# Kernel optimization log

Hardware: AMD Instinct MI355X
Metric: run time of the kernel (lower is better)

The kernel has to match this reference:

```python
import jax, jax.numpy as jnp
import numpy as np
from jax import lax

EPS = 1e-5
DN = ('NCHW', 'OIHW', 'NCHW')

def _sign(v):
    # (v >= 0) * 2 - 1
    return jnp.where(v >= 0, 1.0, -1.0).astype(v.dtype)

def _conv(x, w, b):
    y = lax.conv_general_dilated(x, w, (1, 1), 'VALID', dimension_numbers=DN)
    return y + b[None, :, None, None]

def _bn(x):
    # BatchNorm2d(affine=False), training mode: biased batch stats over (N,H,W)
    m = jnp.mean(x, axis=(0, 2, 3), keepdims=True)
    v = jnp.var(x, axis=(0, 2, 3), keepdims=True)
    return (x - m) * lax.rsqrt(v + EPS)

def setup_inputs() -> dict:
    key = jax.random.key(0)
    ks = jax.random.split(key, 9)
    f = jnp.float32
    B = 8192
    x = jax.random.normal(ks[0], (B, 1, 28, 28), dtype=f)
    # conv params, clipped to [-1, 1] as in clip_weights()
    w1 = jnp.clip(jax.random.normal(ks[1], (32, 1, 9, 9), dtype=f) * 0.1, -1, 1)
    b1 = jnp.clip(jax.random.normal(ks[2], (32,), dtype=f) * 0.1, -1, 1)
    w2 = jnp.clip(jax.random.normal(ks[3], (16, 32, 9, 9), dtype=f) * 0.1, -1, 1)
    b2 = jnp.clip(jax.random.normal(ks[4], (16,), dtype=f) * 0.1, -1, 1)
    w3 = jnp.clip(jax.random.normal(ks[5], (8, 16, 9, 9), dtype=f) * 0.1, -1, 1)
    b3 = jnp.clip(jax.random.normal(ks[6], (8,), dtype=f) * 0.1, -1, 1)
    wl = jnp.clip(jax.random.normal(ks[7], (10, 8, 4, 4), dtype=f) * 0.1, -1, 1)
    bl = jnp.clip(jax.random.normal(ks[8], (10,), dtype=f) * 0.1, -1, 1)
    return {"x": x, "w1": w1, "b1": b1, "w2": w2, "b2": b2,
            "w3": w3, "b3": b3, "wl": wl, "bl": bl}

def _block(x, w, b, act=True, norm=True, binarized=True):
    if binarized:
        w, b = _sign(w), _sign(b)
    x = _conv(x, w, b)
    if norm:
        x = _bn(x)
    if act:
        x = _sign(x) if binarized else jax.nn.relu(x)
    return x

def reference(x, w1, b1, w2, b2, w3, b3, wl, bl):
    x = _sign(x)                        # binarize input activations
    x = _block(x, w1, b1)               # (B, 32, 20, 20)
    x = _block(x, w2, b2)               # (B, 16, 12, 12)
    x = _block(x, w3, b3)               # (B,  8,  4,  4)
    x = _block(x, wl, bl, act=False, norm=False)  # (B, 10, 1, 1), binarized weights
    return x.reshape(-1, 10)
```

## Files before the change

### kernel.cpp

```cpp
#include <hip/hip_runtime.h>
#include <stdint.h>

#define BATCH 8192

#define OFF_W1R3   0
#define OFF_W2P    384
#define OFF_W3P    6144
#define OFF_WLB    9600
#define OFF_SBL    9760
#define OFF_TTOT   9856
#define OFF_S3     10184
#define OFF_S2PART 10496
#define OFF_Z2     76800
#define OFF_Z3     37825792

__global__ __launch_bounds__(256) void k1_pack_tsum(const float* __restrict__ x,
                                                    const float* __restrict__ w1,
                                                    const float* __restrict__ w2,
                                                    const float* __restrict__ w3,
                                                    const float* __restrict__ wl,
                                                    const float* __restrict__ bl,
                                                    uint8_t* __restrict__ ws) {
  int* Ttot = (int*)(ws + OFF_TTOT);
  const int tid = threadIdx.x;

  if (blockIdx.x == 0) {
    uint32_t* W1R3 = (uint32_t*)(ws + OFF_W1R3);
    uint32_t* W2P  = (uint32_t*)(ws + OFF_W2P);
    uint32_t* W3P  = (uint32_t*)(ws + OFF_W3P);
    uint64_t* WLB  = (uint64_t*)(ws + OFF_WLB);
    float*    SBL  = (float*)(ws + OFF_SBL);
    for (int e = tid; e < 96; e += 256) {
      int oc = e / 3, i = e % 3;
      uint32_t m = 0;
      for (int rr = 0; rr < 3; ++rr)
        for (int kw = 0; kw < 9; ++kw)
          if (w1[oc*81 + (3*i+rr)*9 + kw] < 0.f) m |= 1u << (rr*9 + kw);
      W1R3[e] = m;
    }
    for (int e = tid; e < 648; e += 256) {
      int och = e / 81, k = e % 81;
      int kh = k / 9, kw = k % 9;
      uint32_t m0 = 0, m1 = 0;
      int oc0 = och*2;
      for (int ic = 0; ic < 32; ++ic) {
        if (w2[(oc0*32 + ic)*81 + k] < 0.f)     m0 |= 1u << ic;
        if (w2[((oc0+1)*32 + ic)*81 + k] < 0.f) m1 |= 1u << ic;
      }
      int idx = ((och*9 + kh)*10 + kw)*2;
      W2P[idx] = m0; W2P[idx+1] = m1;
    }
    for (int e = tid; e < 72; e += 256) {
      int idx = (e*10 + 9)*2;
      W2P[idx] = 0; W2P[idx+1] = 0;
    }
    for (int e = tid; e < 648; e += 256) {
      int oc = e / 81, k = e % 81;
      int kh = k / 9, kw = k % 9;
      uint32_t m = 0;
      for (int ic = 0; ic < 16; ++ic)
        if (w3[(oc*16 + ic)*81 + k] < 0.f) m |= 1u << ic;
      W3P[(oc*9 + kh)*12 + kw] = m;
    }
    for (int e = tid; e < 216; e += 256) {
      int row = e / 3, p = e % 3;
      W3P[row*12 + 9 + p] = 0;
    }
    for (int e = tid; e < 20; e += 256) {
      int oc = e >> 1, word = e & 1;
      uint64_t m = 0;
      for (int b = 0; b < 64; ++b)
        if (wl[oc*128 + word*64 + b] < 0.f) m |= 1ull << b;
      WLB[e] = m;
    }
    if (tid < 10) SBL[tid] = (bl[tid] >= 0.f) ? 1.f : -1.f;
  }

  __shared__ uint32_t rowm[896];
  __shared__ int Tacc[81];
  if (tid < 81) Tacc[tid] = 0;
  __syncthreads();

  const int img0 = blockIdx.x * 32;
  #pragma unroll
  for (int it = 0; it < 4; ++it) {
    int R = tid + it*256;
    if (R < 896) {
      int il = R / 28, r = R % 28;
      const float4* xr = (const float4*)(x + (size_t)(img0 + il) * 784 + r * 28);
      uint32_t m = 0;
      #pragma unroll
      for (int j = 0; j < 7; ++j) {
        float4 v = xr[j];
        if (v.x < 0.f) m |= 1u << (j*4+0);
        if (v.y < 0.f) m |= 1u << (j*4+1);
        if (v.z < 0.f) m |= 1u << (j*4+2);
        if (v.w < 0.f) m |= 1u << (j*4+3);
      }
      rowm[R] = m;
    }
  }
  __syncthreads();

  for (int T = tid; T < 288; T += 256) {
    int il = T / 9, kw = T % 9;
    int base = il * 28;
    int n9[9];
    int sum20 = 0;
    #pragma unroll
    for (int r = 0; r < 20; ++r) {
      int n = __popc((rowm[base + r] >> kw) & 0xFFFFFu);
      if (r < 9) n9[r] = n;
      sum20 += n;
    }
    atomicAdd(&Tacc[kw], 400 - 2*sum20);
    #pragma unroll
    for (int kh = 1; kh <= 8; ++kh) {
      int nadd = __popc((rowm[base + kh + 19] >> kw) & 0xFFFFFu);
      sum20 += nadd - n9[kh-1];
      atomicAdd(&Tacc[kh*9 + kw], 400 - 2*sum20);
    }
  }
  __syncthreads();
  if (tid < 81) atomicAdd(&Ttot[tid], Tacc[tid]);
}

#define K2_IMGS 8
__global__ __launch_bounds__(256) void k2_conv12(const float* __restrict__ x,
                                                 uint8_t* __restrict__ ws) {
  const uint32_t* W1R3g = (const uint32_t*)(ws + OFF_W1R3);
  const uint32_t* W2Pg  = (const uint32_t*)(ws + OFF_W2P);
  const int* Ttot = (const int*)(ws + OFF_TTOT);
  int* S2P = (int*)(ws + OFF_S2PART);

  __shared__ uint32_t __attribute__((aligned(16))) rowm[K2_IMGS*28];
  __shared__ uint32_t __attribute__((aligned(16))) w1r3[96];
  __shared__ uint32_t __attribute__((aligned(16))) w2p[1440];
  __shared__ int tlds[81];
  __shared__ int t1s[32];
  __shared__ uint32_t __attribute__((aligned(16))) A1s[K2_IMGS*400];
  __shared__ int s2acc[16];

  const int tid = threadIdx.x;
  const int img0 = blockIdx.x * K2_IMGS;

  for (int e = tid; e < 96; e += 256)   w1r3[e] = W1R3g[e];
  for (int e = tid; e < 1440; e += 256) w2p[e]  = W2Pg[e];
  if (tid < 81) tlds[tid] = Ttot[tid];
  if (tid < 16) s2acc[tid] = 0;
  if (tid < K2_IMGS*28) {
    int il = tid / 28, rr = tid % 28;
    const float4* xr = (const float4*)(x + (size_t)(img0 + il) * 784 + rr * 28);
    uint32_t m = 0;
    #pragma unroll
    for (int j = 0; j < 7; ++j) {
      float4 v = xr[j];
      if (v.x < 0.f) m |= 1u << (j*4+0);
      if (v.y < 0.f) m |= 1u << (j*4+1);
      if (v.z < 0.f) m |= 1u << (j*4+2);
      if (v.w < 0.f) m |= 1u << (j*4+3);
    }
    rowm[tid] = m;
  }
  __syncthreads();

  if (tid < 32) {
    long long S = 0;
    for (int kh = 0; kh < 9; ++kh)
      for (int kw = 0; kw < 9; ++kw) {
        int bit = (w1r3[tid*3 + kh/3] >> ((kh%3)*9 + kw)) & 1;
        S += (long long)(1 - 2*bit) * tlds[kh*9 + kw];
      }
    const long long N1 = (long long)BATCH * 400;
    long long q = S / N1, rr = S % N1;
    long long t = q + (rr > 0 ? 1 : 0);
    if ((t & 1) == 0) t += 1;
    t1s[tid] = (int)t;
  }
  __syncthreads();

  for (int G = tid; G < K2_IMGS*80; G += 256) {
    int il = G / 80, rem = G - il*80;
    int oh = rem >> 2, ow0 = (rem & 3) * 5;
    uint32_t R[9];
    #pragma unroll
    for (int i = 0; i < 9; ++i) R[i] = rowm[il*28 + oh + i];
    uint32_t win[5][3];
    #pragma unroll
    for (int j = 0; j < 5; ++j) {
      int ow = ow0 + j;
      #pragma unroll
      for (int i = 0; i < 3; ++i) {
        uint32_t b0 = (R[3*i]   >> ow) & 0x1FFu;
        uint32_t b1 = (R[3*i+1] >> ow) & 0x1FFu;
        uint32_t b2 = (R[3*i+2] >> ow) & 0x1FFu;
        win[j][i] = b0 | (b1 << 9) | (b2 << 18);
      }
    }
    uint32_t mask[5] = {0,0,0,0,0};
    #pragma unroll
    for (int ocg = 0; ocg < 4; ++ocg) {
      const uint4* wp = (const uint4*)&w1r3[ocg*24];
      uint32_t wr[24];
      #pragma unroll
      for (int q = 0; q < 6; ++q) {
        uint4 v = wp[q];
        wr[q*4+0]=v.x; wr[q*4+1]=v.y; wr[q*4+2]=v.z; wr[q*4+3]=v.w;
      }
      #pragma unroll
      for (int o8 = 0; o8 < 8; ++o8) {
        int oc = ocg*8 + o8;
        int t = t1s[oc];
        #pragma unroll
        for (int j = 0; j < 5; ++j) {
          int mm = __popc(win[j][0] ^ wr[o8*3])
                 + __popc(win[j][1] ^ wr[o8*3+1])
                 + __popc(win[j][2] ^ wr[o8*3+2]);
          mask[j] |= (uint32_t)((81 - 2*mm) < t) << oc;
        }
      }
    }
    #pragma unroll
    for (int j = 0; j < 5; ++j) A1s[il*400 + oh*20 + ow0 + j] = mask[j];
  }
  __syncthreads();

  uint32_t* Z2w = (uint32_t*)(ws + OFF_Z2);
  const int och = tid & 7, oc0 = och << 1;
  int sl0 = 0, sl1 = 0;
  for (int r = 0; r < 3; ++r) {
    int G = tid + r*256;
    int il = G / 96, rem = G - il*96;
    int oy = rem >> 3;
    const uint32_t* A = &A1s[il*400 + oy*20];
    int acc0[12], acc1[12];
    #pragma unroll
    for (int p = 0; p < 12; ++p) { acc0[p] = 0; acc1[p] = 0; }
    for (int kh = 0; kh < 9; ++kh) {
      const uint4* ar = (const uint4*)(A + kh*20);
      uint32_t a[20];
      #pragma unroll
      for (int q = 0; q < 5; ++q) {
        uint4 v = ar[q];
        a[q*4+0]=v.x; a[q*4+1]=v.y; a[q*4+2]=v.z; a[q*4+3]=v.w;
      }
      const uint4* wp4 = (const uint4*)&w2p[(och*9 + kh)*20];
      uint32_t wbuf[20];
      #pragma unroll
      for (int q = 0; q < 5; ++q) {
        uint4 v = wp4[q];
        wbuf[q*4+0]=v.x; wbuf[q*4+1]=v.y; wbuf[q*4+2]=v.z; wbuf[q*4+3]=v.w;
      }
      #pragma unroll
      for (int kw = 0; kw < 9; ++kw) {
        uint32_t w0 = wbuf[2*kw], w1v = wbuf[2*kw+1];
        #pragma unroll
        for (int px = 0; px < 12; ++px) {
          acc0[px] += __popc(a[kw+px] ^ w0);
          acc1[px] += __popc(a[kw+px] ^ w1v);
        }
      }
    }
    size_t wbase = (size_t)(img0+il)*1152 + (size_t)oy*96 + och;
    #pragma unroll
    for (int px = 0; px < 12; ++px) {
      int z0 = 2592 - 2*acc0[px], z1v = 2592 - 2*acc1[px];
      sl0 += z0; sl1 += z1v;
      Z2w[wbase + px*8] = (uint32_t)(uint16_t)(int16_t)z0
                        | ((uint32_t)(uint16_t)(int16_t)z1v << 16);
    }
  }
  atomicAdd(&s2acc[oc0],   sl0);
  atomicAdd(&s2acc[oc0+1], sl1);
  __syncthreads();
  if (tid < 16) S2P[blockIdx.x*16 + tid] = s2acc[tid];
}

__global__ __launch_bounds__(256) void k3_conv3(uint8_t* __restrict__ ws) {
  const int* S2P = (const int*)(ws + OFF_S2PART);
  const uint32_t* W3Pg = (const uint32_t*)(ws + OFF_W3P);
  const uint32_t* Z2w = (const uint32_t*)(ws + OFF_Z2);
  uint32_t* Z3w = (uint32_t*)(ws + OFF_Z3);
  unsigned long long* S3 = (unsigned long long*)(ws + OFF_S3);

  __shared__ uint32_t __attribute__((aligned(16))) w3p[864];
  __shared__ int part[256];
  __shared__ int t2s[16];
  __shared__ uint32_t __attribute__((aligned(16))) A2[32*144];
  __shared__ int s3acc[8];

  const int tid = threadIdx.x;
  const int img0 = blockIdx.x * 32;

  {
    int c = tid & 15, g = tid >> 4;
    int s = 0;
    for (int j = 0; j < 64; ++j) s += S2P[(g + 16*j)*16 + c];
    part[tid] = s;
  }
  for (int e = tid; e < 864; e += 256) w3p[e] = W3Pg[e];
  if (tid < 8) s3acc[tid] = 0;
  __syncthreads();
  if (tid < 16) {
    long long S = 0;
    #pragma unroll
    for (int g = 0; g < 16; ++g) S += (long long)part[g*16 + tid];
    const long long N2 = (long long)BATCH * 144;
    long long q = S / N2, r = S % N2;
    long long t = q + (r > 0 ? 1 : 0);
    if (t & 1) t += 1;
    t2s[tid] = (int)t;
  }
  __syncthreads();

  #pragma unroll
  for (int j = 0; j < 18; ++j) {
    int idx = tid + j*256;
    const uint4* zp = (const uint4*)&Z2w[(size_t)(img0 + idx/144)*1152 + (size_t)(idx%144)*8];
    uint4 v0 = zp[0], v1 = zp[1];
    uint32_t zz[8] = {v0.x,v0.y,v0.z,v0.w, v1.x,v1.y,v1.z,v1.w};
    uint32_t m = 0;
    #pragma unroll
    for (int i = 0; i < 8; ++i) {
      int zlo = (int)(short)(zz[i] & 0xFFFFu);
      int zhi = (int)zz[i] >> 16;
      m |= (uint32_t)(zlo < t2s[2*i])   << (2*i);
      m |= (uint32_t)(zhi < t2s[2*i+1]) << (2*i+1);
    }
    A2[idx] = m;
  }
  __syncthreads();

  const int il = tid >> 3, oc = tid & 7;
  int acc[16];
  #pragma unroll
  for (int i = 0; i < 16; ++i) acc[i] = 0;
  #pragma unroll
  for (int r = 0; r < 12; ++r) {
    const uint4* ar = (const uint4*)&A2[il*144 + r*12];
    uint4 v0 = ar[0], v1 = ar[1], v2 = ar[2];
    uint32_t a[12] = {v0.x,v0.y,v0.z,v0.w, v1.x,v1.y,v1.z,v1.w, v2.x,v2.y,v2.z,v2.w};
    #pragma unroll
    for (int oy = 0; oy < 4; ++oy) {
      if (r - oy >= 0 && r - oy <= 8) {
        int kh = r - oy;
        const uint4* wr = (const uint4*)&w3p[(oc*9 + kh)*12];
        uint4 w0 = wr[0], w1v = wr[1], w2v = wr[2];
        uint32_t w[9] = {w0.x,w0.y,w0.z,w0.w, w1v.x,w1v.y,w1v.z,w1v.w, w2v.x};
        #pragma unroll
        for (int ox = 0; ox < 4; ++ox) {
          int m = 0;
          #pragma unroll
          for (int kw = 0; kw < 9; ++kw) m += __popc(a[ox+kw] ^ w[kw]);
          acc[oy*4+ox] += m;
        }
      }
    }
  }
  int ssum = 0;
  uint32_t packed[8];
  #pragma unroll
  for (int h = 0; h < 8; ++h) {
    int za = 1296 - 2*acc[2*h], zb = 1296 - 2*acc[2*h+1];
    ssum += za + zb;
    packed[h] = (uint32_t)(uint16_t)(int16_t)za | ((uint32_t)(uint16_t)(int16_t)zb << 16);
  }
  uint4* zp = (uint4*)&Z3w[(size_t)(img0 + il)*64 + oc*8];
  zp[0] = make_uint4(packed[0], packed[1], packed[2], packed[3]);
  zp[1] = make_uint4(packed[4], packed[5], packed[6], packed[7]);
  atomicAdd(&s3acc[oc], ssum);
  __syncthreads();
  if (tid < 8)
    atomicAdd(&S3[tid], (unsigned long long)(long long)s3acc[tid]);
}

__global__ __launch_bounds__(256) void k4_final(uint8_t* __restrict__ ws,
                                                float* __restrict__ out) {
  const uint32_t* Z3w = (const uint32_t*)(ws + OFF_Z3);
  const long long* S3 = (const long long*)(ws + OFF_S3);
  const uint64_t* WLBg = (const uint64_t*)(ws + OFF_WLB);
  const float* SBLg = (const float*)(ws + OFF_SBL);
  __shared__ int t3[8];
  __shared__ uint64_t wlb[20];
  __shared__ float sbl[10];
  const int tid = threadIdx.x;
  if (tid < 8) {
    long long S = S3[tid];
    const long long N3 = (long long)BATCH * 16;
    long long q = S / N3, r = S % N3;
    long long t = q + (r > 0 ? 1 : 0);
    if (t & 1) t += 1;
    t3[tid] = (int)t;
  }
  if (tid < 20) wlb[tid] = WLBg[tid];
  if (tid < 10) sbl[tid] = SBLg[tid];
  __syncthreads();
  int img = blockIdx.x * 256 + tid;
  const uint4* zp = (const uint4*)&Z3w[(size_t)img * 64];
  uint32_t zz[64];
  #pragma unroll
  for (int q = 0; q < 16; ++q) {
    uint4 v = zp[q];
    zz[q*4+0]=v.x; zz[q*4+1]=v.y; zz[q*4+2]=v.z; zz[q*4+3]=v.w;
  }
  uint64_t a0 = 0, a1 = 0;
  #pragma unroll
  for (int j = 0; j < 64; ++j) {
    int z = (j & 1) ? ((int)zz[j>>1] >> 16) : (int)(short)(zz[j>>1] & 0xFFFFu);
    a0 |= (uint64_t)(z < t3[j >> 4]) << j;
  }
  #pragma unroll
  for (int j = 0; j < 64; ++j) {
    int z = (j & 1) ? ((int)zz[32 + (j>>1)] >> 16) : (int)(short)(zz[32 + (j>>1)] & 0xFFFFu);
    a1 |= (uint64_t)(z < t3[(64 + j) >> 4]) << j;
  }
  #pragma unroll
  for (int oc = 0; oc < 10; ++oc) {
    int mism = __popcll(a0 ^ wlb[oc*2]) + __popcll(a1 ^ wlb[oc*2 + 1]);
    out[(size_t)img*10 + oc] = (float)(128 - 2*mism) + sbl[oc];
  }
}

extern "C" void kernel_launch(void* const* d_in, const int* in_sizes, int n_in,
                              void* d_out, int out_size, void* d_ws, size_t ws_size,
                              hipStream_t stream) {
  (void)in_sizes; (void)n_in; (void)out_size; (void)ws_size;
  const float* x  = (const float*)d_in[0];
  const float* w1 = (const float*)d_in[1];
  const float* w2 = (const float*)d_in[3];
  const float* w3 = (const float*)d_in[5];
  const float* wl = (const float*)d_in[7];
  const float* bl = (const float*)d_in[8];
  uint8_t* ws = (uint8_t*)d_ws;
  float* out = (float*)d_out;

  hipMemsetAsync(ws + OFF_TTOT, 0, 400, stream);
  k1_pack_tsum<<<256, 256, 0, stream>>>(x, w1, w2, w3, wl, bl, ws);
  k2_conv12<<<1024, 256, 0, stream>>>(x, ws);
  k3_conv3<<<256, 256, 0, stream>>>(ws);
  k4_final<<<32, 256, 0, stream>>>(ws, out);
}
```

Baseline: 257.8 us.

## Spread k1, k3 and k4 across more blocks with smaller per-block work

Cuts images per block in k1 and k3 from 32 to 8 and quadruples their grid to 1024 blocks. k3 now gives each thread one output row (oy) instead of a whole 4x4 tile, which removes the redundant row-loop masking and shrinks the register accumulators. k4 drops to 64-thread blocks across 128 blocks. The aim is to fill more compute units on a GPU with many CUs. In exchange, per-block overheads such as the S2P partial reduction in k3, the weight packing and the shared/global atomics are repeated across more blocks.

```diff
diff --git a/kernel.cpp b/kernel.cpp
--- a/kernel.cpp
+++ b/kernel.cpp
@@ -76,34 +76,30 @@
     if (tid < 10) SBL[tid] = (bl[tid] >= 0.f) ? 1.f : -1.f;
   }
 
-  __shared__ uint32_t rowm[896];
+  __shared__ uint32_t rowm[224];
   __shared__ int Tacc[81];
   if (tid < 81) Tacc[tid] = 0;
   __syncthreads();
 
-  const int img0 = blockIdx.x * 32;
-  #pragma unroll
-  for (int it = 0; it < 4; ++it) {
-    int R = tid + it*256;
-    if (R < 896) {
-      int il = R / 28, r = R % 28;
-      const float4* xr = (const float4*)(x + (size_t)(img0 + il) * 784 + r * 28);
-      uint32_t m = 0;
-      #pragma unroll
-      for (int j = 0; j < 7; ++j) {
-        float4 v = xr[j];
-        if (v.x < 0.f) m |= 1u << (j*4+0);
-        if (v.y < 0.f) m |= 1u << (j*4+1);
-        if (v.z < 0.f) m |= 1u << (j*4+2);
-        if (v.w < 0.f) m |= 1u << (j*4+3);
-      }
-      rowm[R] = m;
-    }
-  }
-  __syncthreads();
-
-  for (int T = tid; T < 288; T += 256) {
-    int il = T / 9, kw = T % 9;
+  const int img0 = blockIdx.x * 8;
+  if (tid < 224) {
+    int il = tid / 28, r = tid % 28;
+    const float4* xr = (const float4*)(x + (size_t)(img0 + il) * 784 + r * 28);
+    uint32_t m = 0;
+    #pragma unroll
+    for (int j = 0; j < 7; ++j) {
+      float4 v = xr[j];
+      if (v.x < 0.f) m |= 1u << (j*4+0);
+      if (v.y < 0.f) m |= 1u << (j*4+1);
+      if (v.z < 0.f) m |= 1u << (j*4+2);
+      if (v.w < 0.f) m |= 1u << (j*4+3);
+    }
+    rowm[tid] = m;
+  }
+  __syncthreads();
+
+  if (tid < 72) {
+    int il = tid / 9, kw = tid % 9;
     int base = il * 28;
     int n9[9];
     int sum20 = 0;
@@ -276,6 +272,7 @@
   if (tid < 16) S2P[blockIdx.x*16 + tid] = s2acc[tid];
 }
 
+#define K3_IMGS 8
 __global__ __launch_bounds__(256) void k3_conv3(uint8_t* __restrict__ ws) {
   const int* S2P = (const int*)(ws + OFF_S2PART);
   const uint32_t* W3Pg = (const uint32_t*)(ws + OFF_W3P);
@@ -286,11 +283,11 @@
   __shared__ uint32_t __attribute__((aligned(16))) w3p[864];
   __shared__ int part[256];
   __shared__ int t2s[16];
-  __shared__ uint32_t __attribute__((aligned(16))) A2[32*144];
+  __shared__ uint32_t __attribute__((aligned(16))) A2[K3_IMGS*144];
   __shared__ int s3acc[8];
 
   const int tid = threadIdx.x;
-  const int img0 = blockIdx.x * 32;
+  const int img0 = blockIdx.x * K3_IMGS;
 
   {
     int c = tid & 15, g = tid >> 4;
@@ -313,9 +310,7 @@
   }
   __syncthreads();
 
-  #pragma unroll
-  for (int j = 0; j < 18; ++j) {
-    int idx = tid + j*256;
+  for (int idx = tid; idx < K3_IMGS*144; idx += 256) {
     const uint4* zp = (const uint4*)&Z2w[(size_t)(img0 + idx/144)*1152 + (size_t)(idx%144)*8];
     uint4 v0 = zp[0], v1 = zp[1];
     uint32_t zz[8] = {v0.x,v0.y,v0.z,v0.w, v1.x,v1.y,v1.z,v1.w};
@@ -331,51 +326,39 @@
   }
   __syncthreads();
 
-  const int il = tid >> 3, oc = tid & 7;
-  int acc[16];
-  #pragma unroll
-  for (int i = 0; i < 16; ++i) acc[i] = 0;
-  #pragma unroll
-  for (int r = 0; r < 12; ++r) {
-    const uint4* ar = (const uint4*)&A2[il*144 + r*12];
+  const int il = tid >> 5, oc = (tid >> 2) & 7, oy = tid & 3;
+  int acc[4] = {0, 0, 0, 0};
+  #pragma unroll
+  for (int kh = 0; kh < 9; ++kh) {
+    const uint4* ar = (const uint4*)&A2[il*144 + (oy + kh)*12];
     uint4 v0 = ar[0], v1 = ar[1], v2 = ar[2];
     uint32_t a[12] = {v0.x,v0.y,v0.z,v0.w, v1.x,v1.y,v1.z,v1.w, v2.x,v2.y,v2.z,v2.w};
-    #pragma unroll
-    for (int oy = 0; oy < 4; ++oy) {
-      if (r - oy >= 0 && r - oy <= 8) {
-        int kh = r - oy;
-        const uint4* wr = (const uint4*)&w3p[(oc*9 + kh)*12];
-        uint4 w0 = wr[0], w1v = wr[1], w2v = wr[2];
-        uint32_t w[9] = {w0.x,w0.y,w0.z,w0.w, w1v.x,w1v.y,w1v.z,w1v.w, w2v.x};
-        #pragma unroll
-        for (int ox = 0; ox < 4; ++ox) {
-          int m = 0;
-          #pragma unroll
-          for (int kw = 0; kw < 9; ++kw) m += __popc(a[ox+kw] ^ w[kw]);
-          acc[oy*4+ox] += m;
-        }
-      }
+    const uint4* wr = (const uint4*)&w3p[(oc*9 + kh)*12];
+    uint4 w0 = wr[0], w1v = wr[1], w2v = wr[2];
+    uint32_t w[9] = {w0.x,w0.y,w0.z,w0.w, w1v.x,w1v.y,w1v.z,w1v.w, w2v.x};
+    #pragma unroll
+    for (int ox = 0; ox < 4; ++ox) {
+      #pragma unroll
+      for (int kw = 0; kw < 9; ++kw) acc[ox] += __popc(a[ox+kw] ^ w[kw]);
     }
   }
   int ssum = 0;
-  uint32_t packed[8];
-  #pragma unroll
-  for (int h = 0; h < 8; ++h) {
+  uint32_t packed[2];
+  #pragma unroll
+  for (int h = 0; h < 2; ++h) {
     int za = 1296 - 2*acc[2*h], zb = 1296 - 2*acc[2*h+1];
     ssum += za + zb;
     packed[h] = (uint32_t)(uint16_t)(int16_t)za | ((uint32_t)(uint16_t)(int16_t)zb << 16);
   }
-  uint4* zp = (uint4*)&Z3w[(size_t)(img0 + il)*64 + oc*8];
-  zp[0] = make_uint4(packed[0], packed[1], packed[2], packed[3]);
-  zp[1] = make_uint4(packed[4], packed[5], packed[6], packed[7]);
+  *(uint2*)&Z3w[(size_t)(img0 + il)*64 + oc*8 + oy*2] = make_uint2(packed[0], packed[1]);
   atomicAdd(&s3acc[oc], ssum);
   __syncthreads();
   if (tid < 8)
     atomicAdd(&S3[tid], (unsigned long long)(long long)s3acc[tid]);
 }
 
-__global__ __launch_bounds__(256) void k4_final(uint8_t* __restrict__ ws,
-                                                float* __restrict__ out) {
+__global__ __launch_bounds__(64) void k4_final(uint8_t* __restrict__ ws,
+                                               float* __restrict__ out) {
   const uint32_t* Z3w = (const uint32_t*)(ws + OFF_Z3);
   const long long* S3 = (const long long*)(ws + OFF_S3);
   const uint64_t* WLBg = (const uint64_t*)(ws + OFF_WLB);
@@ -395,7 +378,7 @@
   if (tid < 20) wlb[tid] = WLBg[tid];
   if (tid < 10) sbl[tid] = SBLg[tid];
   __syncthreads();
-  int img = blockIdx.x * 256 + tid;
+  int img = blockIdx.x * 64 + tid;
   const uint4* zp = (const uint4*)&Z3w[(size_t)img * 64];
   uint32_t zz[64];
   #pragma unroll
@@ -435,8 +418,8 @@
   float* out = (float*)d_out;
 
   hipMemsetAsync(ws + OFF_TTOT, 0, 400, stream);
-  k1_pack_tsum<<<256, 256, 0, stream>>>(x, w1, w2, w3, wl, bl, ws);
+  k1_pack_tsum<<<1024, 256, 0, stream>>>(x, w1, w2, w3, wl, bl, ws);
   k2_conv12<<<1024, 256, 0, stream>>>(x, ws);
-  k3_conv3<<<256, 256, 0, stream>>>(ws);
-  k4_final<<<32, 256, 0, stream>>>(ws, out);
+  k3_conv3<<<1024, 256, 0, stream>>>(ws);
+  k4_final<<<128, 64, 0, stream>>>(ws, out);
 }
```

New measurement: 272.4 us. +5.6%, slower.
